# Kernel optimization log

Hardware: AMD Instinct MI355X
Metric: run time of the kernel (lower is better)

The kernel has to match this reference:

```python
import jax, jax.numpy as jnp
import numpy as np

N, L, D, F, NUM_BAGS = 262144, 1024, 128, 32, 256


def setup_inputs() -> dict:
    key = jax.random.key(0)
    ks = jax.random.split(key, 12)
    x = jax.random.normal(ks[0], (N, L), dtype=jnp.float32)
    idxs = jnp.sort(jax.random.randint(ks[1], (N,), 0, NUM_BAGS, dtype=jnp.int64))
    def lin(k, fan_in, fan_out):
        s = 1.0 / np.sqrt(fan_in)
        return jax.random.uniform(k, (fan_in, fan_out), jnp.float32, -s, s)
    W1 = lin(ks[2], L, D);  b1 = jnp.zeros((D,), jnp.float32)
    Wt = lin(ks[3], D, F);  bt = jnp.zeros((F,), jnp.float32)
    Ws = lin(ks[4], D, F);  bs = jnp.zeros((F,), jnp.float32)
    Wa = lin(ks[5], F, 1);  ba = jnp.zeros((1,), jnp.float32)
    Wp = lin(ks[6], D, F);  bp = jnp.zeros((F,), jnp.float32)
    return {"x": x, "idxs": idxs, "W1": W1, "b1": b1, "Wt": Wt, "bt": bt,
            "Ws": Ws, "bs": bs, "Wa": Wa, "ba": ba, "Wp": Wp, "bp": bp}


def reference(x, idxs, W1, b1, Wt, bt, Ws, bs, Wa, ba, Wp, bp):
    # feature extractor (Dropout is identity at eval time)
    H = jax.nn.relu(x @ W1 + b1)                       # [N, D]
    # gated attention scores
    At = jnp.tanh(H @ Wt + bt)                         # [N, F]
    As = jax.nn.sigmoid(H @ Ws + bs)                   # [N, F]
    a = ((At * As) @ Wa + ba)[:, 0]                    # [N]
    # per-bag (segment) softmax, numerically stable
    amax = jax.ops.segment_max(a, idxs, num_segments=NUM_BAGS)   # [B]
    w = jnp.exp(a - amax[idxs])                         # [N]
    den = jax.ops.segment_sum(w, idxs, num_segments=NUM_BAGS)    # [B]
    w = w / den[idxs]
    # segment weighted reduce: M[b] = sum_i w_i * H_i over bag b
    M = jax.ops.segment_sum(w[:, None] * H, idxs, num_segments=NUM_BAGS)  # [B, D]
    # projector + L2 normalize (torch F.normalize eps=1e-12)
    proj = M @ Wp + bp                                  # [B, F]
    nrm = jnp.maximum(jnp.linalg.norm(proj, axis=1, keepdims=True), 1e-12)
    proj = proj / nrm
    return M, proj
```

## Files before the change

kernel.cpp:

```cpp
#include <hip/hip_runtime.h>
#include <hip/hip_bf16.h>

#define NTOT 262144
#define LDIM 1024
#define DDIM 128
#define FDIM 32
#define NBAGS 256

typedef __attribute__((ext_vector_type(8))) short bf16x8;
typedef __attribute__((ext_vector_type(4))) float f32x4;

__device__ __forceinline__ unsigned short f2b(float f) {
    __hip_bfloat16 h = __float2bfloat16(f);
    return __builtin_bit_cast(unsigned short, h);
}
__device__ __forceinline__ float b2f(unsigned short u) {
    union { float f; unsigned int i; } c;
    c.i = ((unsigned int)u) << 16;
    return c.f;
}

__global__ void k_prep(const float* __restrict__ W1, ushort* __restrict__ w1t2,
                       float* __restrict__ Mraw, float* __restrict__ dden) {
    int gid = blockIdx.x * 256 + threadIdx.x;
    if (gid < LDIM * DDIM) {
        int col = gid & 127, k = gid >> 7;
        int kt = k >> 6, ko = k & 63;
        int cc = ko >> 3, kr = ko & 7;
        int ccs = cc ^ (col & 7);
        w1t2[kt * 8192 + col * 64 + ccs * 8 + kr] = f2b(W1[gid]);
    }
    if (gid < NBAGS * DDIM) Mraw[gid] = 0.0f;
    if (gid < NBAGS) dden[gid] = 0.0f;
}

__global__ __launch_bounds__(256, 3) void k_fused_gemm(
    const float* __restrict__ x, const ushort* __restrict__ w1t2,
    const float* __restrict__ b1,
    const float* __restrict__ Wt, const float* __restrict__ bt,
    const float* __restrict__ Ws, const float* __restrict__ bs,
    const float* __restrict__ Wa, const float* __restrict__ ba,
    const int* __restrict__ idxs,
    float* __restrict__ Mraw, float* __restrict__ dden)
{
    __shared__ __align__(16) ushort sAB[16384];
    __shared__ __align__(16) ushort sWtT[4096];
    __shared__ __align__(16) ushort sWsT[4096];
    __shared__ float sb1[128];
    __shared__ float sbt[32], sbs[32], sWa[32];
    __shared__ float sw[128];
    __shared__ int   sbag[128];

    const int t    = threadIdx.x;
    const int lane = t & 63;
    const int wave = t >> 6;
    const int wr   = wave >> 1, wc = wave & 1;
    const int lq   = lane >> 4, lr = lane & 15;
    const int row0 = blockIdx.x * 128;

    for (int e = t; e < 4096; e += 256) {
        int d = e >> 5, f = e & 31;
        int byt = f * 256 + ((((d >> 3) ^ (f & 15))) << 4) + (d & 7) * 2;
        *(ushort*)((char*)sWtT + byt) = f2b(Wt[e]);
        *(ushort*)((char*)sWsT + byt) = f2b(Ws[e]);
    }
    if (t < 128) { sb1[t] = b1[t]; sbag[t] = idxs[row0 + t]; }
    if (t < 32)  { sbt[t] = bt[t]; sbs[t] = bs[t]; sWa[t] = Wa[t]; }
    const float ba0 = ba[0];

    f32x4 acc[4][4];
#pragma unroll
    for (int m = 0; m < 4; ++m)
#pragma unroll
        for (int n = 0; n < 4; ++n) acc[m][n] = 0;

    char* sA = (char*)sAB;
    char* sB = (char*)sAB + 16384;

    const int arow  = t >> 4;
    const int acol4 = (t & 15) * 4;
    const float* xb = x + (size_t)(row0 + arow) * LDIM + acol4;
    const int a_base = (((acol4 >> 3) ^ (arow & 7)) << 4) + (acol4 & 7) * 2;
    const ushort* bb = w1t2 + t * 8;
    char* sBw = sB + t * 16;

    float4 av[8];
    bf16x8 bv[4];
#pragma unroll
    for (int j = 0; j < 8; ++j) av[j] = *(const float4*)(xb + j * (16 * LDIM));
#pragma unroll
    for (int jj = 0; jj < 4; ++jj) bv[jj] = *(const bf16x8*)(bb + jj * 2048);

    for (int kt = 0; kt < 16; ++kt) {
        __syncthreads();

#pragma unroll
        for (int j = 0; j < 8; ++j) {
            float4 f = av[j];
            uint2 pk;
            pk.x = (unsigned)f2b(f.x) | ((unsigned)f2b(f.y) << 16);
            pk.y = (unsigned)f2b(f.z) | ((unsigned)f2b(f.w) << 16);
            *(uint2*)(sA + (arow + 16 * j) * 128 + a_base) = pk;
        }
#pragma unroll
        for (int jj = 0; jj < 4; ++jj)
            *(bf16x8*)(sBw + jj * 4096) = bv[jj];
        __syncthreads();

        if (kt < 15) {
            const float* xk = xb + (kt + 1) * 64;
#pragma unroll
            for (int j = 0; j < 8; ++j) av[j] = *(const float4*)(xk + j * (16 * LDIM));
            const ushort* bk = bb + (kt + 1) * 8192;
#pragma unroll
            for (int jj = 0; jj < 4; ++jj) bv[jj] = *(const bf16x8*)(bk + jj * 2048);
        }

#pragma unroll
        for (int kk = 0; kk < 2; ++kk) {
            bf16x8 aF[4], bF[4];
#pragma unroll
            for (int m = 0; m < 4; ++m) {
                int ra = wr * 64 + m * 16 + lr;
                aF[m] = *(const bf16x8*)(sA + ra * 128 + (((kk * 4 + lq) ^ (ra & 7)) << 4));
            }
#pragma unroll
            for (int n = 0; n < 4; ++n) {
                int cb = wc * 64 + n * 16 + lr;
                bF[n] = *(const bf16x8*)(sB + cb * 128 + (((kk * 4 + lq) ^ (cb & 7)) << 4));
            }
#pragma unroll
            for (int m = 0; m < 4; ++m)
#pragma unroll
                for (int n = 0; n < 4; ++n)
                    acc[m][n] = __builtin_amdgcn_mfma_f32_16x16x32_bf16(aF[m], bF[n], acc[m][n], 0, 0, 0);
        }
    }
    __syncthreads();

    char* sH = (char*)sAB;
#pragma unroll
    for (int m = 0; m < 4; ++m) {
#pragma unroll
        for (int n = 0; n < 4; ++n) {
            const int colg = wc * 64 + n * 16 + lr;
            const float bias = sb1[colg];
#pragma unroll
            for (int r = 0; r < 4; ++r) {
                const int rowl = wr * 64 + m * 16 + lq * 4 + r;
                float h = acc[m][n][r] + bias;
                h = fmaxf(h, 0.0f);
                *(ushort*)(sH + rowl * 256 + (((colg >> 3) ^ (rowl & 15)) << 4) + (colg & 7) * 2) = f2b(h);
            }
        }
    }
    __syncthreads();

    {
        f32x4 at_[2][2], as_[2][2];
#pragma unroll
        for (int m = 0; m < 2; ++m)
#pragma unroll
            for (int n = 0; n < 2; ++n) { at_[m][n] = 0; as_[m][n] = 0; }

        const char* cWtT = (const char*)sWtT;
        const char* cWsT = (const char*)sWsT;
#pragma unroll
        for (int kk = 0; kk < 4; ++kk) {
            bf16x8 aH[2], bT[2], bS[2];
            const int slot = kk * 4 + lq;
#pragma unroll
            for (int m = 0; m < 2; ++m) {
                const int ra = wave * 32 + m * 16 + lr;
                aH[m] = *(const bf16x8*)(sH + ra * 256 + ((slot ^ (ra & 15)) << 4));
            }
#pragma unroll
            for (int n = 0; n < 2; ++n) {
                const int f = n * 16 + lr;
                bT[n] = *(const bf16x8*)(cWtT + f * 256 + ((slot ^ (f & 15)) << 4));
                bS[n] = *(const bf16x8*)(cWsT + f * 256 + ((slot ^ (f & 15)) << 4));
            }
#pragma unroll
            for (int m = 0; m < 2; ++m)
#pragma unroll
                for (int n = 0; n < 2; ++n) {
                    at_[m][n] = __builtin_amdgcn_mfma_f32_16x16x32_bf16(aH[m], bT[n], at_[m][n], 0, 0, 0);
                    as_[m][n] = __builtin_amdgcn_mfma_f32_16x16x32_bf16(aH[m], bS[n], as_[m][n], 0, 0, 0);
                }
        }

#pragma unroll
        for (int m = 0; m < 2; ++m) {
#pragma unroll
            for (int r = 0; r < 4; ++r) {
                float s = 0.f;
#pragma unroll
                for (int n = 0; n < 2; ++n) {
                    const int f = n * 16 + lr;
                    float tv = tanhf(at_[m][n][r] + sbt[f]);
                    float sg = 1.0f / (1.0f + __expf(-(as_[m][n][r] + sbs[f])));
                    s += tv * sg * sWa[f];
                }
                s += __shfl_xor(s, 1);
                s += __shfl_xor(s, 2);
                s += __shfl_xor(s, 4);
                s += __shfl_xor(s, 8);
                if (lr == 0)
                    sw[wave * 32 + m * 16 + lq * 4 + r] = __expf(s + ba0);
            }
        }
    }
    __syncthreads();

    {
        const int d = t & 127, half = t >> 7;
        const int r0 = half * 64;
        float accv = 0.f, accw = 0.f;
        int curbag = sbag[r0];
        for (int r = 0; r < 64; ++r) {
            const int rr = r0 + r;
            const int bg = sbag[rr];
            if (bg != curbag) {
                atomicAdd(&Mraw[curbag * 128 + d], accv);
                if (d == 0) atomicAdd(&dden[curbag], accw);
                accv = 0.f; accw = 0.f; curbag = bg;
            }
            const float w = sw[rr];
            const ushort hv = *(const ushort*)(sH + rr * 256 + ((((d >> 3) ^ (rr & 15))) << 4) + (d & 7) * 2);
            accv += w * b2f(hv);
            accw += w;
        }
        atomicAdd(&Mraw[curbag * 128 + d], accv);
        if (d == 0) atomicAdd(&dden[curbag], accw);
    }
}

__global__ __launch_bounds__(128) void k_final(
    const float* __restrict__ Mraw, const float* __restrict__ dden,
    const float* __restrict__ Wp, const float* __restrict__ bp,
    float* __restrict__ out)
{
    __shared__ float sM[128];
    const int b = blockIdx.x, t = threadIdx.x;
    const float den = dden[b];
    const float inv_den = den > 0.f ? 1.0f / den : 0.0f;

    float m = Mraw[b * 128 + t] * inv_den;
    sM[t] = m;
    out[b * 128 + t] = m;
    __syncthreads();

    if (t < 32) {
        float p = bp[t];
        for (int d = 0; d < 128; ++d) p += sM[d] * Wp[d * 32 + t];
        float ss = p * p;
#pragma unroll
        for (int mm = 1; mm < 32; mm <<= 1) ss += __shfl_xor(ss, mm);
        float nrm = sqrtf(ss);
        out[32768 + b * 32 + t] = p / fmaxf(nrm, 1e-12f);
    }
}

extern "C" void kernel_launch(void* const* d_in, const int* in_sizes, int n_in,
                              void* d_out, int out_size, void* d_ws, size_t ws_size,
                              hipStream_t stream)
{
    const float* x  = (const float*)d_in[0];
    const int*   idxs = (const int*)d_in[1];
    const float* W1 = (const float*)d_in[2];
    const float* b1 = (const float*)d_in[3];
    const float* Wt = (const float*)d_in[4];
    const float* bt = (const float*)d_in[5];
    const float* Ws = (const float*)d_in[6];
    const float* bs = (const float*)d_in[7];
    const float* Wa = (const float*)d_in[8];
    const float* ba = (const float*)d_in[9];
    const float* Wp = (const float*)d_in[10];
    const float* bp = (const float*)d_in[11];
    float* out = (float*)d_out;

    char* ws = (char*)d_ws;
    float*  Mraw = (float*)ws;
    float*  dden = (float*)(ws + 131072);
    ushort* w1t2 = (ushort*)(ws + 132096);

    k_prep<<<512, 256, 0, stream>>>(W1, w1t2, Mraw, dden);
    k_fused_gemm<<<2048, 256, 0, stream>>>(x, w1t2, b1, Wt, bt, Ws, bs, Wa, ba, idxs, Mraw, dden);
    k_final<<<NBAGS, 128, 0, stream>>>(Mraw, dden, Wp, bp, out);
}
```

Before: 231.8 us.

## Read W1 and gate weights directly from global memory instead of staging in LDS

The prep kernel now writes W1 as a plain transposed bf16 matrix and also pre-converts Wt/Ws to transposed bf16 in the workspace. The fused GEMM loads B fragments for the main GEMM and the attention GEMMs straight from global/L2 rather than staging them through shared memory. This removes the LDS footprint and stores for B and the per-block Wt/Ws conversion, allowing occupancy to go from 3 to 4 blocks. In exchange, every wave issues uncoalesced-ish global loads each k-step that depend on L2 hit rates and are no longer prefetched ahead.

After: 269.6 us. 1.16x slower.

```diff
diff --git a/kernel.cpp b/kernel.cpp
--- a/kernel.cpp
+++ b/kernel.cpp
@@ -20,32 +20,35 @@
     return c.f;
 }
 
-__global__ void k_prep(const float* __restrict__ W1, ushort* __restrict__ w1t2,
+__global__ void k_prep(const float* __restrict__ W1, const float* __restrict__ Wt,
+                       const float* __restrict__ Ws,
+                       ushort* __restrict__ w1t, ushort* __restrict__ wtT,
+                       ushort* __restrict__ wsT,
                        float* __restrict__ Mraw, float* __restrict__ dden) {
     int gid = blockIdx.x * 256 + threadIdx.x;
     if (gid < LDIM * DDIM) {
         int col = gid & 127, k = gid >> 7;
-        int kt = k >> 6, ko = k & 63;
-        int cc = ko >> 3, kr = ko & 7;
-        int ccs = cc ^ (col & 7);
-        w1t2[kt * 8192 + col * 64 + ccs * 8 + kr] = f2b(W1[gid]);
+        w1t[col * 1024 + k] = f2b(W1[gid]);
+    }
+    if (gid < DDIM * FDIM) {
+        int f = gid & 31, d = gid >> 5;
+        wtT[f * 128 + d] = f2b(Wt[gid]);
+        wsT[f * 128 + d] = f2b(Ws[gid]);
     }
     if (gid < NBAGS * DDIM) Mraw[gid] = 0.0f;
     if (gid < NBAGS) dden[gid] = 0.0f;
 }
 
-__global__ __launch_bounds__(256, 3) void k_fused_gemm(
-    const float* __restrict__ x, const ushort* __restrict__ w1t2,
+__global__ __launch_bounds__(256, 4) void k_fused_gemm(
+    const float* __restrict__ x, const ushort* __restrict__ w1t,
+    const ushort* __restrict__ wtT, const ushort* __restrict__ wsT,
     const float* __restrict__ b1,
-    const float* __restrict__ Wt, const float* __restrict__ bt,
-    const float* __restrict__ Ws, const float* __restrict__ bs,
+    const float* __restrict__ bt, const float* __restrict__ bs,
     const float* __restrict__ Wa, const float* __restrict__ ba,
     const int* __restrict__ idxs,
     float* __restrict__ Mraw, float* __restrict__ dden)
 {
     __shared__ __align__(16) ushort sAB[16384];
-    __shared__ __align__(16) ushort sWtT[4096];
-    __shared__ __align__(16) ushort sWsT[4096];
     __shared__ float sb1[128];
     __shared__ float sbt[32], sbs[32], sWa[32];
     __shared__ float sw[128];
@@ -58,12 +61,6 @@
     const int lq   = lane >> 4, lr = lane & 15;
     const int row0 = blockIdx.x * 128;
 
-    for (int e = t; e < 4096; e += 256) {
-        int d = e >> 5, f = e & 31;
-        int byt = f * 256 + ((((d >> 3) ^ (f & 15))) << 4) + (d & 7) * 2;
-        *(ushort*)((char*)sWtT + byt) = f2b(Wt[e]);
-        *(ushort*)((char*)sWsT + byt) = f2b(Ws[e]);
-    }
     if (t < 128) { sb1[t] = b1[t]; sbag[t] = idxs[row0 + t]; }
     if (t < 32)  { sbt[t] = bt[t]; sbs[t] = bs[t]; sWa[t] = Wa[t]; }
     const float ba0 = ba[0];
@@ -75,21 +72,16 @@
         for (int n = 0; n < 4; ++n) acc[m][n] = 0;
 
     char* sA = (char*)sAB;
-    char* sB = (char*)sAB + 16384;
 
     const int arow  = t >> 4;
     const int acol4 = (t & 15) * 4;
     const float* xb = x + (size_t)(row0 + arow) * LDIM + acol4;
     const int a_base = (((acol4 >> 3) ^ (arow & 7)) << 4) + (acol4 & 7) * 2;
-    const ushort* bb = w1t2 + t * 8;
-    char* sBw = sB + t * 16;
+    const ushort* wb = w1t + (size_t)(wc * 64 + lr) * 1024;
 
     float4 av[8];
-    bf16x8 bv[4];
 #pragma unroll
     for (int j = 0; j < 8; ++j) av[j] = *(const float4*)(xb + j * (16 * LDIM));
-#pragma unroll
-    for (int jj = 0; jj < 4; ++jj) bv[jj] = *(const bf16x8*)(bb + jj * 2048);
 
     for (int kt = 0; kt < 16; ++kt) {
         __syncthreads();
@@ -102,18 +94,12 @@
             pk.y = (unsigned)f2b(f.z) | ((unsigned)f2b(f.w) << 16);
             *(uint2*)(sA + (arow + 16 * j) * 128 + a_base) = pk;
         }
-#pragma unroll
-        for (int jj = 0; jj < 4; ++jj)
-            *(bf16x8*)(sBw + jj * 4096) = bv[jj];
         __syncthreads();
 
         if (kt < 15) {
             const float* xk = xb + (kt + 1) * 64;
 #pragma unroll
             for (int j = 0; j < 8; ++j) av[j] = *(const float4*)(xk + j * (16 * LDIM));
-            const ushort* bk = bb + (kt + 1) * 8192;
-#pragma unroll
-            for (int jj = 0; jj < 4; ++jj) bv[jj] = *(const bf16x8*)(bk + jj * 2048);
         }
 
 #pragma unroll
@@ -125,10 +111,8 @@
                 aF[m] = *(const bf16x8*)(sA + ra * 128 + (((kk * 4 + lq) ^ (ra & 7)) << 4));
             }
 #pragma unroll
-            for (int n = 0; n < 4; ++n) {
-                int cb = wc * 64 + n * 16 + lr;
-                bF[n] = *(const bf16x8*)(sB + cb * 128 + (((kk * 4 + lq) ^ (cb & 7)) << 4));
-            }
+            for (int n = 0; n < 4; ++n)
+                bF[n] = *(const bf16x8*)(wb + n * 16384 + kt * 64 + kk * 32 + lq * 8);
 #pragma unroll
             for (int m = 0; m < 4; ++m)
 #pragma unroll
@@ -163,8 +147,6 @@
 #pragma unroll
             for (int n = 0; n < 2; ++n) { at_[m][n] = 0; as_[m][n] = 0; }
 
-        const char* cWtT = (const char*)sWtT;
-        const char* cWsT = (const char*)sWsT;
 #pragma unroll
         for (int kk = 0; kk < 4; ++kk) {
             bf16x8 aH[2], bT[2], bS[2];
@@ -177,8 +159,8 @@
 #pragma unroll
             for (int n = 0; n < 2; ++n) {
                 const int f = n * 16 + lr;
-                bT[n] = *(const bf16x8*)(cWtT + f * 256 + ((slot ^ (f & 15)) << 4));
-                bS[n] = *(const bf16x8*)(cWsT + f * 256 + ((slot ^ (f & 15)) << 4));
+                bT[n] = *(const bf16x8*)(wtT + f * 128 + kk * 32 + lq * 8);
+                bS[n] = *(const bf16x8*)(wsT + f * 128 + kk * 32 + lq * 8);
             }
 #pragma unroll
             for (int m = 0; m < 2; ++m)
@@ -282,9 +264,11 @@
     char* ws = (char*)d_ws;
     float*  Mraw = (float*)ws;
     float*  dden = (float*)(ws + 131072);
-    ushort* w1t2 = (ushort*)(ws + 132096);
-
-    k_prep<<<512, 256, 0, stream>>>(W1, w1t2, Mraw, dden);
-    k_fused_gemm<<<2048, 256, 0, stream>>>(x, w1t2, b1, Wt, bt, Ws, bs, Wa, ba, idxs, Mraw, dden);
+    ushort* w1t  = (ushort*)(ws + 132096);
+    ushort* wtT  = (ushort*)(ws + 132096 + 262144);
+    ushort* wsT  = (ushort*)(ws + 132096 + 262144 + 8192);
+
+    k_prep<<<512, 256, 0, stream>>>(W1, Wt, Ws, w1t, wtT, wsT, Mraw, dden);
+    k_fused_gemm<<<2048, 256, 0, stream>>>(x, w1t, wtT, wsT, b1, bt, bs, Wa, ba, idxs, Mraw, dden);
     k_final<<<NBAGS, 128, 0, stream>>>(Mraw, dden, Wp, bp, out);
 }
```
